# Kernel tuning notes

Hardware: AMD Instinct MI355X
Metric: run time of the kernel (lower is better)

The kernel has to match this reference:

```python
import jax, jax.numpy as jnp
import numpy as np

DIM = 2048
NUM_HEADS = 16
HEAD_DIM = DIM // NUM_HEADS  # 128


def setup_inputs() -> dict:
    key = jax.random.key(0)
    ks = jax.random.split(key, 5)
    scale = 0.02
    x = jax.random.normal(ks[0], (1, 2048, DIM), dtype=jnp.float32)
    # nn.Linear weights stored as [out_features, in_features]
    Wq = jax.random.normal(ks[1], (DIM, DIM), dtype=jnp.float32) * scale
    Wk = jax.random.normal(ks[2], (HEAD_DIM, DIM), dtype=jnp.float32) * scale
    Wv = jax.random.normal(ks[3], (HEAD_DIM, DIM), dtype=jnp.float32) * scale
    Wo = jax.random.normal(ks[4], (DIM, DIM), dtype=jnp.float32) * scale
    return {"x": x, "Wq": Wq, "Wk": Wk, "Wv": Wv, "Wo": Wo}


def reference(x, Wq, Wk, Wv, Wo):
    batch, seq_len, dim = x.shape
    q = x @ Wq.T                                   # [b, s, dim]
    k = x @ Wk.T                                   # [b, s, head_dim] (shared across heads)
    v = x @ Wv.T                                   # [b, s, head_dim]
    q = q.reshape(batch, seq_len, NUM_HEADS, HEAD_DIM).transpose(0, 2, 1, 3)  # [b, h, s, d]
    # MQA: single KV head broadcast across query heads (no materialized repeat)
    scores = jnp.einsum("bhqd,bkd->bhqk", q, k) / (HEAD_DIM ** 0.5)
    probs = jax.nn.softmax(scores, axis=-1)        # [b, h, q, k]
    out = jnp.einsum("bhqk,bkd->bhqd", probs, v)   # [b, h, s, d]
    out = out.transpose(0, 2, 1, 3).reshape(batch, seq_len, dim)
    return out @ Wo.T
```

## Files before the change

### kernel.cpp

```cpp
#include <hip/hip_runtime.h>

typedef float  float4_t __attribute__((ext_vector_type(4)));
typedef __bf16 bf16x8   __attribute__((ext_vector_type(8)));
typedef unsigned short u16;

__device__ __forceinline__ u16 f2bf(float f) {
    unsigned u = __float_as_uint(f);
    u += 0x7fffu + ((u >> 16) & 1u);
    return (u16)(u >> 16);
}

#define GLOAD_LDS16(g, l)                                              \
    __builtin_amdgcn_global_load_lds(                                  \
        (__attribute__((address_space(1))) void*)(g),                  \
        (__attribute__((address_space(3))) void*)(l), 16, 0, 0)

__global__ __launch_bounds__(256) void cast_all(const float* __restrict__ x,
                                                const float* __restrict__ wq,
                                                const float* __restrict__ wk,
                                                const float* __restrict__ wv,
                                                const float* __restrict__ wo,
                                                u16* __restrict__ xb, u16* __restrict__ wqb,
                                                u16* __restrict__ wkb, u16* __restrict__ wvb,
                                                u16* __restrict__ wob) {
    const int b = blockIdx.x;
    const float* src;
    u16* dst;
    int i;
    if (b < 4096)      { src = x;  dst = xb;  i = b * 256 + threadIdx.x; }
    else if (b < 8192) { src = wq; dst = wqb; i = (b - 4096) * 256 + threadIdx.x; }
    else if (b < 8448) { src = wk; dst = wkb; i = (b - 8192) * 256 + threadIdx.x; }
    else if (b < 8704) { src = wv; dst = wvb; i = (b - 8448) * 256 + threadIdx.x; }
    else               { src = wo; dst = wob; i = (b - 8704) * 256 + threadIdx.x; }
    float4 f = ((const float4*)src)[i];
    ushort4 r;
    r.x = f2bf(f.x); r.y = f2bf(f.y); r.z = f2bf(f.z); r.w = f2bf(f.w);
    ((ushort4*)dst)[i] = r;
}

template <typename EPI>
__device__ __forceinline__ void gemm_core(const u16* __restrict__ A,
                                          const u16* __restrict__ B,
                                          int K, int bm, int bn, EPI epi) {
    __shared__ __align__(16) u16 As[64 * 32];
    __shared__ __align__(16) u16 Bs[128 * 32];
    const int tid  = threadIdx.x;
    const int lane = tid & 63, wave = tid >> 6;
    const int quad = lane >> 4, l16 = lane & 15;

    float4_t acc[4][2] = {};
    const int r0 = tid >> 2;
    const int c0 = (tid & 3) * 8;

    for (int k0 = 0; k0 < K; k0 += 32) {
        GLOAD_LDS16(A + (size_t)(bm + r0) * K + k0 + c0, &As[tid * 8]);
#pragma unroll
        for (int i = 0; i < 2; ++i) {
            const int slot = i * 256 + tid;
            const int row  = slot >> 2, ch = (slot & 3) * 8;
            GLOAD_LDS16(B + (size_t)(bn + row) * K + k0 + ch, &Bs[slot * 8]);
        }
        __syncthreads();

        bf16x8 af[4], bfr[2];
#pragma unroll
        for (int mi = 0; mi < 4; ++mi)
            af[mi] = *(const bf16x8*)&As[(mi * 16 + l16) * 32 + quad * 8];
#pragma unroll
        for (int ni = 0; ni < 2; ++ni)
            bfr[ni] = *(const bf16x8*)&Bs[(wave * 32 + ni * 16 + l16) * 32 + quad * 8];
#pragma unroll
        for (int mi = 0; mi < 4; ++mi)
#pragma unroll
            for (int ni = 0; ni < 2; ++ni)
                acc[mi][ni] = __builtin_amdgcn_mfma_f32_16x16x32_bf16(
                    af[mi], bfr[ni], acc[mi][ni], 0, 0, 0);
        __syncthreads();
    }

#pragma unroll
    for (int mi = 0; mi < 4; ++mi) {
        const int row = bm + mi * 16 + quad * 4;
#pragma unroll
        for (int ni = 0; ni < 2; ++ni) {
            const int col = bn + wave * 32 + ni * 16 + l16;
#pragma unroll
            for (int r = 0; r < 4; ++r) epi(row + r, col, acc[mi][ni][r]);
        }
    }
}

__global__ __launch_bounds__(256) void gemm_qkv(const u16* __restrict__ A,
                                                const u16* __restrict__ B,
                                                u16* __restrict__ qb,
                                                u16* __restrict__ kb,
                                                u16* __restrict__ vtb) {
    gemm_core(A, B, 2048, blockIdx.x * 64, blockIdx.y * 128,
              [=](int row, int col, float v) {
                  if (col < 2048)
                      qb[(size_t)row * 2048 + col] = f2bf(v * 0.08838834764831845f);
                  else if (col < 2176)
                      kb[(size_t)row * 128 + (col - 2048)] = f2bf(v);
                  else
                      vtb[(size_t)(col - 2176) * 2048 + row] = f2bf(v);
              });
}

__global__ __launch_bounds__(256) void gemm_out(const u16* __restrict__ A,
                                                const u16* __restrict__ B,
                                                float* __restrict__ C) {
    gemm_core(A, B, 2048, blockIdx.x * 64, blockIdx.y * 128,
              [=](int row, int col, float v) {
                  C[(size_t)row * 2048 + col] = v;
              });
}

__global__ __launch_bounds__(128) void mqa_attn(const u16* __restrict__ Q,
                                                const u16* __restrict__ Kmat,
                                                const u16* __restrict__ Vt,
                                                float* __restrict__ Oacc0,
                                                float* __restrict__ Oacc1,
                                                float* __restrict__ Lsum) {
    __shared__ __align__(16) u16 Ks[4 * 32 * 32];
    __shared__ __align__(16) u16 Vts[128 * 32];
    __shared__ __align__(16) u16 Ps[2][32 * 40];
    const int tid  = threadIdx.x;
    const int wave = tid >> 6, lane = tid & 63;
    const int quad = lane >> 4, l16 = lane & 15;
    const int h     = blockIdx.y;
    const int ks    = blockIdx.z;
    const int qbase = blockIdx.x * 64 + wave * 32;
    const int kbase = ks * 1024;

    bf16x8 qf[2][4];
#pragma unroll
    for (int mt = 0; mt < 2; ++mt)
#pragma unroll
        for (int kb4 = 0; kb4 < 4; ++kb4)
            qf[mt][kb4] = *(const bf16x8*)(Q + (size_t)(qbase + mt * 16 + l16) * 2048 +
                                           h * 128 + kb4 * 32 + quad * 8);

    float4_t acc[2][8];
#pragma unroll
    for (int mt = 0; mt < 2; ++mt)
#pragma unroll
        for (int nt = 0; nt < 8; ++nt) acc[mt][nt] = (float4_t){0.f, 0.f, 0.f, 0.f};
    float lsum[8] = {};

    u16* pb = Ps[wave];

    for (int s = 0; s < 32; ++s) {
        const int k0 = kbase + s * 32;
#pragma unroll
        for (int i = 0; i < 4; ++i) {
            const int slot = i * 128 + tid;
            const int kb4 = slot >> 7, win = slot & 127;
            const int row = win >> 2, ch = (win & 3) * 8;
            GLOAD_LDS16(Kmat + (size_t)(k0 + row) * 128 + kb4 * 32 + ch, &Ks[slot * 8]);
        }
#pragma unroll
        for (int i = 0; i < 4; ++i) {
            const int slot = i * 128 + tid;
            const int d = slot >> 2, ch = (slot & 3) * 8;
            GLOAD_LDS16(Vt + (size_t)d * 2048 + k0 + ch, &Vts[slot * 8]);
        }
        __syncthreads();

#pragma unroll
        for (int ct = 0; ct < 2; ++ct) {
            float4_t s0 = (float4_t){0.f, 0.f, 0.f, 0.f};
            float4_t s1 = (float4_t){0.f, 0.f, 0.f, 0.f};
#pragma unroll
            for (int kb4 = 0; kb4 < 4; ++kb4) {
                bf16x8 kf = *(const bf16x8*)&Ks[kb4 * 1024 + (ct * 16 + l16) * 32 + quad * 8];
                s0 = __builtin_amdgcn_mfma_f32_16x16x32_bf16(qf[0][kb4], kf, s0, 0, 0, 0);
                s1 = __builtin_amdgcn_mfma_f32_16x16x32_bf16(qf[1][kb4], kf, s1, 0, 0, 0);
            }
#pragma unroll
            for (int r = 0; r < 4; ++r) {
                const float e0 = __expf(s0[r]);
                const float e1 = __expf(s1[r]);
                lsum[r]     += e0;
                lsum[4 + r] += e1;
                pb[(quad * 4 + r) * 40 + ct * 16 + l16]      = f2bf(e0);
                pb[(16 + quad * 4 + r) * 40 + ct * 16 + l16] = f2bf(e1);
            }
        }
        bf16x8 pa[2];
#pragma unroll
        for (int mt = 0; mt < 2; ++mt)
            pa[mt] = *(const bf16x8*)&pb[(mt * 16 + l16) * 40 + quad * 8];
#pragma unroll
        for (int nt = 0; nt < 8; ++nt) {
            bf16x8 vf = *(const bf16x8*)&Vts[(nt * 16 + l16) * 32 + quad * 8];
            acc[0][nt] = __builtin_amdgcn_mfma_f32_16x16x32_bf16(pa[0], vf, acc[0][nt], 0, 0, 0);
            acc[1][nt] = __builtin_amdgcn_mfma_f32_16x16x32_bf16(pa[1], vf, acc[1][nt], 0, 0, 0);
        }
        __syncthreads();
    }

    float* __restrict__ Op = ks ? Oacc1 : Oacc0;
#pragma unroll
    for (int mt = 0; mt < 2; ++mt)
#pragma unroll
        for (int r = 0; r < 4; ++r) {
            const int row = qbase + mt * 16 + quad * 4 + r;
            const size_t base = ((size_t)h * 2048 + row) * 128;
            float lrow = lsum[mt * 4 + r];
#pragma unroll
            for (int off = 1; off < 16; off <<= 1) lrow += __shfl_xor(lrow, off);
            if (l16 == 0) Lsum[(size_t)ks * 32768 + h * 2048 + row] = lrow;
#pragma unroll
            for (int nt = 0; nt < 8; ++nt)
                Op[base + nt * 16 + l16] = acc[mt][nt][r];
        }
}

__global__ __launch_bounds__(256) void attn_combine(const float* __restrict__ O0,
                                                    const float* __restrict__ O1,
                                                    const float* __restrict__ L,
                                                    u16* __restrict__ attn) {
    const int f = blockIdx.x * 256 + threadIdx.x;
    const int d4 = f & 31, h = (f >> 5) & 15, q = f >> 9;
    const int li = h * 2048 + q;
    const float inv = 1.0f / (L[li] + L[32768 + li]);
    const int oi = li * 32 + d4;
    const float4 a = ((const float4*)O0)[oi];
    const float4 b = ((const float4*)O1)[oi];
    ushort4 r;
    r.x = f2bf((a.x + b.x) * inv);
    r.y = f2bf((a.y + b.y) * inv);
    r.z = f2bf((a.z + b.z) * inv);
    r.w = f2bf((a.w + b.w) * inv);
    ((ushort4*)attn)[f] = r;
}

extern "C" void kernel_launch(void* const* d_in, const int* in_sizes, int n_in,
                              void* d_out, int out_size, void* d_ws, size_t ws_size,
                              hipStream_t stream) {
    const float* x  = (const float*)d_in[0];
    const float* Wq = (const float*)d_in[1];
    const float* Wk = (const float*)d_in[2];
    const float* Wv = (const float*)d_in[3];
    const float* Wo = (const float*)d_in[4];
    float* out = (float*)d_out;

    u16* ws   = (u16*)d_ws;
    u16* xb   = ws;
    u16* Wqb  = xb  + (4 << 20);
    u16* Wkb  = Wqb + (4 << 20);
    u16* Wvb  = Wkb + (256 << 10);
    u16* Wob  = Wvb + (256 << 10);
    u16* qb   = Wob + (4 << 20);
    u16* kb   = qb  + (4 << 20);
    u16* vtb  = kb  + (256 << 10);
    u16* attn = vtb + (256 << 10);
    float* Oacc0 = (float*)ws;
    float* Oacc1 = (float*)(attn + (4 << 20));
    float* Lsum  = Oacc1 + (4 << 20);

    cast_all<<<12800, 256, 0, stream>>>(x, Wq, Wk, Wv, Wo, xb, Wqb, Wkb, Wvb, Wob);

    gemm_qkv<<<dim3(32, 18), 256, 0, stream>>>(xb, Wqb, qb, kb, vtb);
    mqa_attn<<<dim3(32, 16, 2), 128, 0, stream>>>(qb, kb, vtb, Oacc0, Oacc1, Lsum);
    attn_combine<<<4096, 256, 0, stream>>>(Oacc0, Oacc1, Lsum, attn);
    gemm_out<<<dim3(32, 16), 256, 0, stream>>>(attn, Wob, out);
}
```

Measured before the change: 240.9 us.

## Deepen GEMM K-step, widen attention blocks to four waves, use exp2

The shared GEMM core now loads a 64-wide K slice per iteration, which halves the number of barrier pairs and doubles the MFMA work between syncs. It also doubles LDS use. The attention kernel now runs four waves per block over 128 queries, so each K/V tile load is shared by more waves and fewer blocks are launched. The exponent switches to exp2f, with log2(e) folded into the Q scale in the QKV epilogue. Fewer blocks (512) on a large GPU may lower occupancy and parallelism.

```diff
diff --git a/kernel.cpp b/kernel.cpp
--- a/kernel.cpp
+++ b/kernel.cpp
@@ -1,4 +1,5 @@
 #include <hip/hip_runtime.h>
+#include <cmath>
 
 typedef float  float4_t __attribute__((ext_vector_type(4)));
 typedef __bf16 bf16x8   __attribute__((ext_vector_type(8)));
@@ -42,39 +43,50 @@
 __device__ __forceinline__ void gemm_core(const u16* __restrict__ A,
                                           const u16* __restrict__ B,
                                           int K, int bm, int bn, EPI epi) {
-    __shared__ __align__(16) u16 As[64 * 32];
-    __shared__ __align__(16) u16 Bs[128 * 32];
+    __shared__ __align__(16) u16 As[2 * 64 * 32];
+    __shared__ __align__(16) u16 Bs[2 * 128 * 32];
     const int tid  = threadIdx.x;
     const int lane = tid & 63, wave = tid >> 6;
     const int quad = lane >> 4, l16 = lane & 15;
 
     float4_t acc[4][2] = {};
-    const int r0 = tid >> 2;
-    const int c0 = (tid & 3) * 8;
-
-    for (int k0 = 0; k0 < K; k0 += 32) {
-        GLOAD_LDS16(A + (size_t)(bm + r0) * K + k0 + c0, &As[tid * 8]);
+
+    for (int k0 = 0; k0 < K; k0 += 64) {
 #pragma unroll
         for (int i = 0; i < 2; ++i) {
             const int slot = i * 256 + tid;
-            const int row  = slot >> 2, ch = (slot & 3) * 8;
-            GLOAD_LDS16(B + (size_t)(bn + row) * K + k0 + ch, &Bs[slot * 8]);
-        }
-        __syncthreads();
-
-        bf16x8 af[4], bfr[2];
+            const int ks = slot >> 8, win = slot & 255;
+            const int row = win >> 2, ch = (win & 3) * 8;
+            GLOAD_LDS16(A + (size_t)(bm + row) * K + k0 + ks * 32 + ch, &As[slot * 8]);
+        }
+#pragma unroll
+        for (int i = 0; i < 4; ++i) {
+            const int slot = i * 256 + tid;
+            const int ks = slot >> 9, win = slot & 511;
+            const int row = win >> 2, ch = (win & 3) * 8;
+            GLOAD_LDS16(B + (size_t)(bn + row) * K + k0 + ks * 32 + ch, &Bs[slot * 8]);
+        }
+        __syncthreads();
+
+        bf16x8 af[2][4], bfr[2][2];
+#pragma unroll
+        for (int ks = 0; ks < 2; ++ks) {
+#pragma unroll
+            for (int mi = 0; mi < 4; ++mi)
+                af[ks][mi] = *(const bf16x8*)&As[ks * 2048 + (mi * 16 + l16) * 32 + quad * 8];
+#pragma unroll
+            for (int ni = 0; ni < 2; ++ni)
+                bfr[ks][ni] = *(const bf16x8*)&Bs[ks * 4096 + (wave * 32 + ni * 16 + l16) * 32 + quad * 8];
+        }
 #pragma unroll
         for (int mi = 0; mi < 4; ++mi)
-            af[mi] = *(const bf16x8*)&As[(mi * 16 + l16) * 32 + quad * 8];
-#pragma unroll
-        for (int ni = 0; ni < 2; ++ni)
-            bfr[ni] = *(const bf16x8*)&Bs[(wave * 32 + ni * 16 + l16) * 32 + quad * 8];
-#pragma unroll
-        for (int mi = 0; mi < 4; ++mi)
-#pragma unroll
-            for (int ni = 0; ni < 2; ++ni)
+#pragma unroll
+            for (int ni = 0; ni < 2; ++ni) {
                 acc[mi][ni] = __builtin_amdgcn_mfma_f32_16x16x32_bf16(
-                    af[mi], bfr[ni], acc[mi][ni], 0, 0, 0);
+                    af[0][mi], bfr[0][ni], acc[mi][ni], 0, 0, 0);
+                acc[mi][ni] = __builtin_amdgcn_mfma_f32_16x16x32_bf16(
+                    af[1][mi], bfr[1][ni], acc[mi][ni], 0, 0, 0);
+            }
         __syncthreads();
     }
 
@@ -98,7 +110,7 @@
     gemm_core(A, B, 2048, blockIdx.x * 64, blockIdx.y * 128,
               [=](int row, int col, float v) {
                   if (col < 2048)
-                      qb[(size_t)row * 2048 + col] = f2bf(v * 0.08838834764831845f);
+                      qb[(size_t)row * 2048 + col] = f2bf(v * 0.1275174313451427f);
                   else if (col < 2176)
                       kb[(size_t)row * 128 + (col - 2048)] = f2bf(v);
                   else
@@ -115,7 +127,7 @@
               });
 }
 
-__global__ __launch_bounds__(128) void mqa_attn(const u16* __restrict__ Q,
+__global__ __launch_bounds__(256) void mqa_attn(const u16* __restrict__ Q,
                                                 const u16* __restrict__ Kmat,
                                                 const u16* __restrict__ Vt,
                                                 float* __restrict__ Oacc0,
@@ -123,13 +135,13 @@
                                                 float* __restrict__ Lsum) {
     __shared__ __align__(16) u16 Ks[4 * 32 * 32];
     __shared__ __align__(16) u16 Vts[128 * 32];
-    __shared__ __align__(16) u16 Ps[2][32 * 40];
+    __shared__ __align__(16) u16 Ps[4][32 * 40];
     const int tid  = threadIdx.x;
     const int wave = tid >> 6, lane = tid & 63;
     const int quad = lane >> 4, l16 = lane & 15;
     const int h     = blockIdx.y;
     const int ks    = blockIdx.z;
-    const int qbase = blockIdx.x * 64 + wave * 32;
+    const int qbase = blockIdx.x * 128 + wave * 32;
     const int kbase = ks * 1024;
 
     bf16x8 qf[2][4];
@@ -152,15 +164,15 @@
     for (int s = 0; s < 32; ++s) {
         const int k0 = kbase + s * 32;
 #pragma unroll
-        for (int i = 0; i < 4; ++i) {
-            const int slot = i * 128 + tid;
+        for (int i = 0; i < 2; ++i) {
+            const int slot = i * 256 + tid;
             const int kb4 = slot >> 7, win = slot & 127;
             const int row = win >> 2, ch = (win & 3) * 8;
             GLOAD_LDS16(Kmat + (size_t)(k0 + row) * 128 + kb4 * 32 + ch, &Ks[slot * 8]);
         }
 #pragma unroll
-        for (int i = 0; i < 4; ++i) {
-            const int slot = i * 128 + tid;
+        for (int i = 0; i < 2; ++i) {
+            const int slot = i * 256 + tid;
             const int d = slot >> 2, ch = (slot & 3) * 8;
             GLOAD_LDS16(Vt + (size_t)d * 2048 + k0 + ch, &Vts[slot * 8]);
         }
@@ -178,8 +190,8 @@
             }
 #pragma unroll
             for (int r = 0; r < 4; ++r) {
-                const float e0 = __expf(s0[r]);
-                const float e1 = __expf(s1[r]);
+                const float e0 = exp2f(s0[r]);
+                const float e1 = exp2f(s1[r]);
                 lsum[r]     += e0;
                 lsum[4 + r] += e1;
                 pb[(quad * 4 + r) * 40 + ct * 16 + l16]      = f2bf(e0);
@@ -262,7 +274,7 @@
     cast_all<<<12800, 256, 0, stream>>>(x, Wq, Wk, Wv, Wo, xb, Wqb, Wkb, Wvb, Wob);
 
     gemm_qkv<<<dim3(32, 18), 256, 0, stream>>>(xb, Wqb, qb, kb, vtb);
-    mqa_attn<<<dim3(32, 16, 2), 128, 0, stream>>>(qb, kb, vtb, Oacc0, Oacc1, Lsum);
+    mqa_attn<<<dim3(16, 16, 2), 256, 0, stream>>>(qb, kb, vtb, Oacc0, Oacc1, Lsum);
     attn_combine<<<4096, 256, 0, stream>>>(Oacc0, Oacc1, Lsum, attn);
     gemm_out<<<dim3(32, 16), 256, 0, stream>>>(attn, Wob, out);
 }
```

Result: faster. 235.8 us (-2.2%).
